# Performance work log

Hardware: AMD Instinct MI355X
Metric: run time of the kernel (lower is better)

Reference implementation:

```python
import jax, jax.numpy as jnp
import numpy as np

T = 4096      # tokens (flattened batch*seq)
DIN = 2048    # input hidden dim
DQ = 2048     # q output dim
DKV = 2048    # per-head-group kv output dim (== DQ here, MHA)
NA = 4        # number of adapters (LoRA/delta models)
R = 16        # lora rank per q/k/v


def setup_inputs() -> dict:
    key = jax.random.key(0)
    ks = jax.random.split(key, 8)
    def rn(k, shape, scale):
        return jax.random.normal(k, shape, dtype=jnp.float32) * scale
    return {
        "x": rn(ks[0], (T, DIN), 1.0),
        "W_base": rn(ks[1], (DQ + 2 * DKV, DIN), DIN ** -0.5),
        "A_buffer_qkv": rn(ks[2], (NA, DIN, 3 * R), DIN ** -0.5),
        "B_buffer_q": rn(ks[3], (NA, R, DQ), R ** -0.5),
        "B_buffer_kv": rn(ks[4], (NA, R, 2 * DKV), R ** -0.5),
        "DeltaW_q": rn(ks[5], (NA, DIN, DQ), DIN ** -0.5),
        "DeltaW_kv": rn(ks[6], (NA, DIN, 2 * DKV), DIN ** -0.5),
        "weight_indices": jax.random.randint(ks[7], (T,), 0, NA, dtype=jnp.int32),
    }


def _ldmm(indices, x, A, B, D):
    """Per-token adapter-indexed (LoRA + dense delta) matmul.
    indices: [T] int, x: [T, din], A: [na, din, r], B: [na, r, dout], D: [na, din, dout].
    out[t] = (x[t] @ A[a]) @ B[a] + x[t] @ D[a]  with a = indices[t].
    Implemented as masked GEMMs over the small fixed adapter set.
    """
    na = A.shape[0]
    out = jnp.zeros((x.shape[0], B.shape[2]), dtype=x.dtype)
    for a in range(na):  # small fixed loop over adapters
        xa = jnp.where((indices == a)[:, None], x, jnp.zeros((), x.dtype))
        out = out + (xa @ A[a]) @ B[a] + xa @ D[a]
    return out


def reference(x, W_base, A_buffer_qkv, B_buffer_q, B_buffer_kv,
              DeltaW_q, DeltaW_kv, weight_indices):
    # base QKV projection (ColumnParallelLinear, no bias): [T, dq + 2*dkv]
    base = x @ W_base.T
    rank = A_buffer_qkv.shape[2] // 3
    b_dim_q = B_buffer_q.shape[2]
    b_dim_kv = B_buffer_kv.shape[2] // 2
    d_dim_kv = DeltaW_kv.shape[2] // 2
    for i in range(3):  # q, k, v slices
        if i == 0:
            o = _ldmm(weight_indices, x,
                      A_buffer_qkv[:, :, :rank], B_buffer_q, DeltaW_q)
            base = base.at[:, :b_dim_q].add(o)
        else:
            o = _ldmm(weight_indices, x,
                      A_buffer_qkv[:, :, i * rank:(i + 1) * rank],
                      B_buffer_kv[:, :, (i - 1) * b_dim_kv:i * b_dim_kv],
                      DeltaW_kv[:, :, (i - 1) * d_dim_kv:i * d_dim_kv])
            base = base.at[:, i * b_dim_kv:(i + 1) * b_dim_kv].add(o)
    return base
```

## Files before the change

kernel.cpp:

```cpp
#include <hip/hip_runtime.h>
#include <stdint.h>

#define T_TOK 4096
#define DIN   2048
#define DQ    2048
#define DKV   2048
#define NOUT  (DQ + 2*DKV)
#define NA    4
#define RLORA 16
#define BM    256
#define BN    256
#define MPAD  (T_TOK + NA*BM)
#define MTILES (MPAD/BM)
#define KX    (DIN + 64)
#define NKT64 (KX/64)
#define KSPLIT 16
#define NTBLK (NOUT/BN)
#define NWG   (MTILES*NTBLK)

typedef unsigned short u16;
typedef __attribute__((ext_vector_type(8))) short short8;
typedef __attribute__((ext_vector_type(8))) u16 u16x8;
typedef __attribute__((ext_vector_type(4))) float f32x4;

__device__ __forceinline__ u16 f2bf(float f) {
  uint32_t u = __float_as_uint(f);
  u = (u + 0x7FFFu + ((u >> 16) & 1u)) >> 16;
  return (u16)u;
}
__device__ __forceinline__ float bf2f(u16 u) {
  return __uint_as_float(((uint32_t)u) << 16);
}

typedef __attribute__((address_space(3))) void lds_void;
typedef __attribute__((address_space(1))) void glb_void;

__device__ __forceinline__ void gl_lds16(const void* g, void* l) {
  __builtin_amdgcn_global_load_lds((const glb_void*)(uintptr_t)g,
                                   (lds_void*)(uint32_t)(uintptr_t)l, 16, 0, 0);
}

__global__ void prep_kernel(const int* __restrict__ widx,
                            int* __restrict__ tok,
                            int* __restrict__ tileAdapter) {
  __shared__ int cnt[256][NA];
  __shared__ int total[NA];
  __shared__ int pad_off[NA];
  const int tid = threadIdx.x;
  const int CH = T_TOK / 256;
  const int base = tid * CH;
  int c[NA] = {0, 0, 0, 0};
  for (int i = 0; i < CH; i++) c[widx[base + i]]++;
  for (int a = 0; a < NA; a++) cnt[tid][a] = c[a];
  __syncthreads();
  if (tid < NA) {
    int s = 0;
    for (int i = 0; i < 256; i++) { int v = cnt[i][tid]; cnt[i][tid] = s; s += v; }
    total[tid] = s;
  }
  __syncthreads();
  if (tid == 0) {
    int off = 0;
    for (int a = 0; a < NA; a++) {
      pad_off[a] = off;
      int ntile = (total[a] + BM - 1) / BM;
      for (int tl = 0; tl < ntile; tl++) tileAdapter[off / BM + tl] = a;
      off += ntile * BM;
    }
    for (int tl = off / BM; tl < MTILES; tl++) tileAdapter[tl] = -1;
  }
  __syncthreads();
  for (int i = tid; i < MPAD; i += 256) tok[i] = -1;
  __syncthreads();
  int myoff[NA];
  for (int a = 0; a < NA; a++) myoff[a] = pad_off[a] + cnt[tid][a];
  for (int i = 0; i < CH; i++) {
    int a = widx[base + i];
    tok[myoff[a]++] = base + i;
  }
}

__global__ void gather_kernel(const float* __restrict__ x,
                              const int* __restrict__ tok,
                              u16* __restrict__ Xg) {
  const int row = blockIdx.x;
  const int t = tok[row];
  const int tid = threadIdx.x;
  u16x8* dst = (u16x8*)(Xg + (size_t)row * KX);
  if (t < 0) {
    u16x8 z = {0, 0, 0, 0, 0, 0, 0, 0};
    dst[tid] = z;
    return;
  }
  const f32x4* src = (const f32x4*)(x + (size_t)t * DIN);
  f32x4 v0 = src[tid * 2];
  f32x4 v1 = src[tid * 2 + 1];
  u16x8 o;
  o[0] = f2bf(v0[0]); o[1] = f2bf(v0[1]); o[2] = f2bf(v0[2]); o[3] = f2bf(v0[3]);
  o[4] = f2bf(v1[0]); o[5] = f2bf(v1[1]); o[6] = f2bf(v1[2]); o[7] = f2bf(v1[3]);
  dst[tid] = o;
}

__global__ __launch_bounds__(256) void xa_partial_kernel(
    const u16* __restrict__ Xg, const float* __restrict__ A_qkv,
    const int* __restrict__ tileAdapter, float* __restrict__ Ppart) {
  const int ks = blockIdx.y;
  const int ad = tileAdapter[blockIdx.x >> 1];
  const int a = ad < 0 ? 0 : ad;
  const int kb = ks * (DIN / KSPLIT);
  const int tid = threadIdx.x;
  const int rg = tid >> 2;
  const int jg = tid & 3;
  const int r0 = blockIdx.x * 128 + rg * 2;
  const int j0 = jg * 12;
  __shared__ float ldsA[64][56];
  float acc[2][12];
  #pragma unroll
  for (int r = 0; r < 2; r++)
    #pragma unroll
    for (int j = 0; j < 12; j++) acc[r][j] = 0.f;

  for (int kc = 0; kc < 2; kc++) {
    const int kbase = kb + kc * 64;
    for (int i = tid; i < 64 * 48; i += 256) {
      int kk = i / 48, j = i - kk * 48;
      ldsA[kk][j] = A_qkv[((size_t)a * DIN + kbase + kk) * (3 * RLORA) + j];
    }
    __syncthreads();
    u16x8 xr[2][8];
    #pragma unroll
    for (int r = 0; r < 2; r++)
      #pragma unroll
      for (int q = 0; q < 8; q++)
        xr[r][q] = *(const u16x8*)(Xg + (size_t)(r0 + r) * KX + kbase + q * 8);
    #pragma unroll
    for (int q = 0; q < 8; q++) {
      #pragma unroll
      for (int e = 0; e < 8; e++) {
        const int kk = q * 8 + e;
        f32x4 a0 = *(const f32x4*)&ldsA[kk][j0];
        f32x4 a1 = *(const f32x4*)&ldsA[kk][j0 + 4];
        f32x4 a2 = *(const f32x4*)&ldsA[kk][j0 + 8];
        float x0 = bf2f(xr[0][q][e]);
        float x1 = bf2f(xr[1][q][e]);
        #pragma unroll
        for (int c = 0; c < 4; c++) {
          acc[0][c]     += x0 * a0[c];  acc[1][c]     += x1 * a0[c];
          acc[0][4 + c] += x0 * a1[c];  acc[1][4 + c] += x1 * a1[c];
          acc[0][8 + c] += x0 * a2[c];  acc[1][8 + c] += x1 * a2[c];
        }
      }
    }
    __syncthreads();
  }
  #pragma unroll
  for (int r = 0; r < 2; r++)
    #pragma unroll
    for (int j = 0; j < 12; j++)
      Ppart[((size_t)ks * MPAD + r0 + r) * 48 + j0 + j] = acc[r][j];
}

__global__ void xa_reduce_kernel(const float* __restrict__ Ppart,
                                 u16* __restrict__ Xg) {
  const int gid = blockIdx.x * 256 + threadIdx.x;
  const int row = gid >> 6, j = gid & 63;
  float s = 0.f;
  if (j < 48) {
    #pragma unroll
    for (int sp = 0; sp < KSPLIT; sp++)
      s += Ppart[((size_t)sp * MPAD + row) * 48 + j];
  }
  Xg[(size_t)row * KX + DIN + j] = f2bf(s);
}

__global__ __launch_bounds__(256) void weff2_kernel(
    const float* __restrict__ W_base,
    const float* __restrict__ DW_q, const float* __restrict__ DW_kv,
    u16* __restrict__ Weff) {
  const int k0 = blockIdx.x * 64;
  const int n0 = blockIdx.y * 64;
  const int tid = threadIdx.x;
  const int k8 = (tid & 7) * 8;
  __shared__ float ldsD[64][65];

  f32x4 wb[2][2];
  #pragma unroll
  for (int h = 0; h < 2; h++) {
    const int nn = h * 32 + (tid >> 3);
    const float* p = W_base + (size_t)(n0 + nn) * DIN + k0 + k8;
    wb[h][0] = *(const f32x4*)p;
    wb[h][1] = *(const f32x4*)(p + 4);
  }

  const int ldD  = (n0 < DQ) ? DQ : 2 * DKV;
  const int ncol = (n0 < DQ) ? n0 : n0 - DQ;
  const float* Dbase = (n0 < DQ) ? (DW_q + ncol) : (DW_kv + ncol);
  const size_t Dstride = (n0 < DQ) ? (size_t)DIN * DQ : (size_t)DIN * (2 * DKV);

  const int lkk = tid >> 6;
  const int lnn = tid & 63;

  float v[16];
  {
    const float* Dp = Dbase;
    #pragma unroll
    for (int j = 0; j < 16; j++)
      v[j] = Dp[(size_t)(k0 + lkk + 4 * j) * ldD + lnn];
  }

  for (int a = 0; a < NA; a++) {
    #pragma unroll
    for (int j = 0; j < 16; j++) ldsD[lkk + 4 * j][lnn] = v[j];
    if (a < NA - 1) {
      const float* Dp = Dbase + (size_t)(a + 1) * Dstride;
      #pragma unroll
      for (int j = 0; j < 16; j++)
        v[j] = Dp[(size_t)(k0 + lkk + 4 * j) * ldD + lnn];
    }
    __syncthreads();
    #pragma unroll
    for (int h = 0; h < 2; h++) {
      const int nn = h * 32 + (tid >> 3);
      u16x8 o;
      #pragma unroll
      for (int j = 0; j < 8; j++)
        o[j] = f2bf(wb[h][j >> 2][j & 3] + ldsD[k8 + j][nn]);
      *(u16x8*)(Weff + ((size_t)a * NOUT + n0 + nn) * KX + k0 + k8) = o;
    }
    __syncthreads();
  }
}

__global__ void wslots_kernel(const float* __restrict__ B_q,
                              const float* __restrict__ B_kv,
                              u16* __restrict__ Weff) {
  const int a = blockIdx.y;
  const int n = blockIdx.x * 256 + threadIdx.x;
  const int seg = n >> 11;
  u16 vals[64];
  #pragma unroll
  for (int j = 0; j < 64; j++) vals[j] = 0;
  if (seg == 0) {
    const float* Bp = B_q + ((size_t)a * RLORA) * DQ + n;
    #pragma unroll
    for (int r = 0; r < RLORA; r++) vals[r] = f2bf(Bp[(size_t)r * DQ]);
  } else if (seg == 1) {
    const float* Bp = B_kv + ((size_t)a * RLORA) * (2 * DKV) + (n - DQ);
    #pragma unroll
    for (int r = 0; r < RLORA; r++) vals[RLORA + r] = f2bf(Bp[(size_t)r * (2 * DKV)]);
  } else {
    const float* Bp = B_kv + ((size_t)a * RLORA) * (2 * DKV) + (n - DQ);
    #pragma unroll
    for (int r = 0; r < RLORA; r++) vals[2 * RLORA + r] = f2bf(Bp[(size_t)r * (2 * DKV)]);
  }
  u16* dst = Weff + ((size_t)a * NOUT + n) * KX + DIN;
  #pragma unroll
  for (int v = 0; v < 8; v++) *(u16x8*)(dst + v * 8) = *(u16x8*)(vals + v * 8);
}

#define BAR      asm volatile("s_barrier" ::: "memory")
#define WAITV(n) asm volatile("s_waitcnt vmcnt(" #n ")" ::: "memory")

#define RD_A(db, mh) { \
  _Pragma("unroll") for (int q = 0; q < 4; ++q) { \
    const char* rp = ldsc + (db)*32768 + (wm*128 + (mh)*64 + q*16 + fr)*128; \
    af[q][0] = *(const short8*)(rp + ck0); \
    af[q][1] = *(const short8*)(rp + ck1); } }

#define RD_B(db, nh, bfv) { \
  _Pragma("unroll") for (int q = 0; q < 2; ++q) { \
    const char* rp = ldsc + 65536 + (db)*32768 + ((nh)*128 + wn*32 + q*16 + fr)*128; \
    bfv[q][0] = *(const short8*)(rp + ck0); \
    bfv[q][1] = *(const short8*)(rp + ck1); } }

#define ST_A(db, mh, t) { \
  gl_lds16(gAsrc + (size_t)((mh)*64)*KX + (size_t)(t)*64, \
           ldsu + (db)*16384 + ((mh)*64*64) + stid); \
  gl_lds16(gAsrc + (size_t)(128 + (mh)*64)*KX + (size_t)(t)*64, \
           ldsu + (db)*16384 + ((128 + (mh)*64)*64) + stid); }

#define ST_B(db, nh, t) { \
  gl_lds16(gBsrc + (size_t)((nh)*32)*KX + (size_t)(t)*64, \
           ldsu + 32768 + (db)*16384 + ((nh)*128*64) + stid); \
  gl_lds16(gBsrc + (size_t)(128 + (nh)*32)*KX + (size_t)(t)*64, \
           ldsu + 32768 + (db)*16384 + (((nh)*128 + 64)*64) + stid); }

#define MM(mh, nh, bfv) { \
  __builtin_amdgcn_s_setprio(1); \
  _Pragma("unroll") for (int q = 0; q < 4; ++q) \
  _Pragma("unroll") for (int r = 0; r < 2; ++r) { \
    acc[(mh)*4+q][(nh)*2+r] = __builtin_amdgcn_mfma_f32_16x16x32_bf16( \
        af[q][0], bfv[r][0], acc[(mh)*4+q][(nh)*2+r], 0, 0, 0); \
    acc[(mh)*4+q][(nh)*2+r] = __builtin_amdgcn_mfma_f32_16x16x32_bf16( \
        af[q][1], bfv[r][1], acc[(mh)*4+q][(nh)*2+r], 0, 0, 0); } \
  __builtin_amdgcn_s_setprio(0); }

#define KT_STD(db, t) { \
  RD_A(db, 0); RD_B(db, 0, bf0); ST_A(1-(db), 1, (t)+1); BAR; MM(0, 0, bf0); BAR; \
  RD_B(db, 1, bf1);              ST_B(1-(db), 0, (t)+1); BAR; MM(0, 1, bf1); BAR; \
  RD_A(db, 1);                   ST_A(db, 0, (t)+2);     BAR; MM(1, 1, bf1); BAR; \
  ST_B(db, 1, (t)+2); WAITV(4);                          BAR; MM(1, 0, bf0); BAR; }

#define KT_T31(db, t) { \
  RD_A(db, 0); RD_B(db, 0, bf0); ST_A(1-(db), 1, (t)+1); BAR; MM(0, 0, bf0); BAR; \
  RD_B(db, 1, bf1);              ST_B(1-(db), 0, (t)+1); BAR; MM(0, 1, bf1); BAR; \
  RD_A(db, 1);                                           BAR; MM(1, 1, bf1); BAR; \
  WAITV(0);                                              BAR; MM(1, 0, bf0); BAR; }

#define KT_LAST(db) { \
  RD_A(db, 0); RD_B(db, 0, bf0); BAR; MM(0, 0, bf0); BAR; \
  RD_B(db, 1, bf1);              BAR; MM(0, 1, bf1); BAR; \
  RD_A(db, 1);                   BAR; MM(1, 1, bf1); BAR; \
                                 BAR; MM(1, 0, bf0); BAR; }

__global__ __launch_bounds__(512, 2) void gemm256_kernel(
    const u16* __restrict__ Xg, const u16* __restrict__ Weff,
    const int* __restrict__ tok, const int* __restrict__ tileAdapter,
    float* __restrict__ out) {
  __shared__ __align__(16) u16 Lds[65536];

  const int bid = blockIdx.x;
  const int lw = (bid & 7) * (NWG / 8) + (bid >> 3);
  const int pg  = lw / (2 * NTBLK);
  const int rem = lw % (2 * NTBLK);
  const int nt  = rem >> 1;
  const int mt  = pg * 2 + (rem & 1);
  const int a = tileAdapter[mt];
  if (a < 0) return;
  const int m0 = mt * BM, n0 = nt * BN;

  const int tid = threadIdx.x;
  const int l = tid & 63, w = tid >> 6;
  const int wm = w >> 2, wn = w & 3;
  const int fr = l & 15;
  const int kq = l >> 4;
  const int s7 = l & 7;
  const int ck0 = ((kq ^ s7) << 4);
  const int ck1 = (((4 + kq) ^ s7) << 4);

  const int l64 = tid >> 3;
  const int swc = (tid & 7) ^ (l64 & 7);
  const int stid = tid * 8;
  const u16* gAsrc = Xg + (size_t)(m0 + l64) * KX + swc * 8;
  const int nB = ((l64 >> 5) * 64) + (l64 & 31);
  const u16* gBsrc = Weff + ((size_t)a * NOUT + n0 + nB) * KX + swc * 8;

  u16* ldsu = &Lds[0];
  const char* ldsc = (const char*)ldsu;

  f32x4 acc[8][4];
  #pragma unroll
  for (int i = 0; i < 8; i++)
    #pragma unroll
    for (int j = 0; j < 4; j++) acc[i][j] = (f32x4){0.f, 0.f, 0.f, 0.f};

  short8 af[4][2], bf0[2][2], bf1[2][2];

  ST_A(0, 0, 0); ST_B(0, 0, 0); ST_A(0, 1, 0); ST_B(0, 1, 0);
  ST_A(1, 0, 1); ST_B(1, 1, 1);
  WAITV(4);
  BAR;

  for (int p = 0; p < 15; ++p) {
    const int t0 = 2 * p;
    KT_STD(0, t0);
    KT_STD(1, t0 + 1);
  }
  KT_STD(0, 30);
  KT_T31(1, 31);
  KT_LAST(0);

  #pragma unroll
  for (int mi = 0; mi < 8; ++mi) {
    const int rb = m0 + wm * 128 + mi * 16 + ((l >> 4) << 2);
    int tt[4];
    #pragma unroll
    for (int reg = 0; reg < 4; ++reg) tt[reg] = tok[rb + reg];
    #pragma unroll
    for (int ni = 0; ni < 4; ++ni) {
      const int col = n0 + wn * 64 + ni * 16 + fr;
      #pragma unroll
      for (int reg = 0; reg < 4; ++reg)
        if (tt[reg] >= 0) out[(size_t)tt[reg] * NOUT + col] = acc[mi][ni][reg];
    }
  }
}

__global__ void fallback_kernel(const float* __restrict__ x,
                                const float* __restrict__ W_base,
                                const float* __restrict__ A_qkv,
                                const float* __restrict__ B_q,
                                const float* __restrict__ B_kv,
                                const float* __restrict__ DW_q,
                                const float* __restrict__ DW_kv,
                                const int* __restrict__ widx,
                                float* __restrict__ out) {
  const int t = blockIdx.x;
  const int n = blockIdx.y * 256 + threadIdx.x;
  const int a = widx[t];
  __shared__ float xs[DIN];
  __shared__ float ys[3 * RLORA];
  for (int k = threadIdx.x; k < DIN; k += 256) xs[k] = x[(size_t)t * DIN + k];
  __syncthreads();
  if (threadIdx.x < 3 * RLORA) {
    float s = 0.f;
    const float* Ap = A_qkv + (size_t)a * DIN * (3 * RLORA) + threadIdx.x;
    for (int k = 0; k < DIN; k++) s += xs[k] * Ap[(size_t)k * (3 * RLORA)];
    ys[threadIdx.x] = s;
  }
  __syncthreads();
  const float* dcol; int ldD, roff; const float* bcol; int ldB;
  if (n < DQ) {
    dcol = DW_q + (size_t)a * DIN * DQ + n; ldD = DQ; roff = 0;
    bcol = B_q + (size_t)a * RLORA * DQ + n; ldB = DQ;
  } else {
    dcol = DW_kv + (size_t)a * DIN * (2 * DKV) + (n - DQ); ldD = 2 * DKV;
    roff = (n < 2 * DQ) ? RLORA : 2 * RLORA;
    bcol = B_kv + (size_t)a * RLORA * (2 * DKV) + (n - DQ); ldB = 2 * DKV;
  }
  const float* wrow = W_base + (size_t)n * DIN;
  float acc = 0.f;
  for (int k = 0; k < DIN; k++) acc += xs[k] * (wrow[k] + dcol[(size_t)k * ldD]);
  for (int r = 0; r < RLORA; r++) acc += ys[roff + r] * bcol[(size_t)r * ldB];
  out[(size_t)t * NOUT + n] = acc;
}

extern "C" void kernel_launch(void* const* d_in, const int* in_sizes, int n_in,
                              void* d_out, int out_size, void* d_ws, size_t ws_size,
                              hipStream_t stream) {
  const float* x      = (const float*)d_in[0];
  const float* W_base = (const float*)d_in[1];
  const float* A_qkv  = (const float*)d_in[2];
  const float* B_q    = (const float*)d_in[3];
  const float* B_kv   = (const float*)d_in[4];
  const float* DW_q   = (const float*)d_in[5];
  const float* DW_kv  = (const float*)d_in[6];
  const int*   widx   = (const int*)d_in[7];
  float* out = (float*)d_out;

  const size_t WEFF_BYTES = (size_t)NA * NOUT * KX * sizeof(u16);
  const size_t XG_BYTES   = (size_t)MPAD * KX * sizeof(u16);
  const size_t TOK_BYTES  = (size_t)MPAD * sizeof(int);
  const size_t TILE_BYTES = (size_t)MTILES * sizeof(int);
  const size_t need = WEFF_BYTES + XG_BYTES + TOK_BYTES + TILE_BYTES;

  if (ws_size < need) {
    fallback_kernel<<<dim3(T_TOK, NOUT / 256), 256, 0, stream>>>(
        x, W_base, A_qkv, B_q, B_kv, DW_q, DW_kv, widx, out);
    return;
  }

  char* ws = (char*)d_ws;
  u16* Weff = (u16*)ws;
  u16* Xg   = (u16*)(ws + WEFF_BYTES);
  int* tok  = (int*)(ws + WEFF_BYTES + XG_BYTES);
  int* tileAdapter = tok + MPAD;
  float* Ppart = (float*)ws;

  prep_kernel<<<1, 256, 0, stream>>>(widx, tok, tileAdapter);
  gather_kernel<<<MPAD, 256, 0, stream>>>(x, tok, Xg);
  xa_partial_kernel<<<dim3(MPAD / 128, KSPLIT), 256, 0, stream>>>(
      Xg, A_qkv, tileAdapter, Ppart);
  xa_reduce_kernel<<<MPAD * 64 / 256, 256, 0, stream>>>(Ppart, Xg);
  weff2_kernel<<<dim3(DIN / 64, NOUT / 64), 256, 0, stream>>>(
      W_base, DW_q, DW_kv, Weff);
  wslots_kernel<<<dim3(NOUT / 256, NA), 256, 0, stream>>>(B_q, B_kv, Weff);
  gemm256_kernel<<<dim3(NWG), 512, 0, stream>>>(
      Xg, Weff, tok, tileAdapter, out);
}
```

Baseline: 249.1 us.

## Switch GEMM main loop to K=32 tiles with 4-stage LDS ring buffer

```diff
diff --git a/kernel.cpp b/kernel.cpp
--- a/kernel.cpp
+++ b/kernel.cpp
@@ -13,7 +13,7 @@
 #define MPAD  (T_TOK + NA*BM)
 #define MTILES (MPAD/BM)
 #define KX    (DIN + 64)
-#define NKT64 (KX/64)
+#define NKT   (KX/32)
 #define KSPLIT 16
 #define NTBLK (NOUT/BN)
 #define NWG   (MTILES*NTBLK)
@@ -261,57 +261,49 @@
 #define BAR      asm volatile("s_barrier" ::: "memory")
 #define WAITV(n) asm volatile("s_waitcnt vmcnt(" #n ")" ::: "memory")
 
-#define RD_A(db, mh) { \
+#define RD_A4(b, mlo) { \
   _Pragma("unroll") for (int q = 0; q < 4; ++q) { \
-    const char* rp = ldsc + (db)*32768 + (wm*128 + (mh)*64 + q*16 + fr)*128; \
-    af[q][0] = *(const short8*)(rp + ck0); \
-    af[q][1] = *(const short8*)(rp + ck1); } }
-
-#define RD_B(db, nh, bfv) { \
-  _Pragma("unroll") for (int q = 0; q < 2; ++q) { \
-    const char* rp = ldsc + 65536 + (db)*32768 + ((nh)*128 + wn*32 + q*16 + fr)*128; \
-    bfv[q][0] = *(const short8*)(rp + ck0); \
-    bfv[q][1] = *(const short8*)(rp + ck1); } }
-
-#define ST_A(db, mh, t) { \
-  gl_lds16(gAsrc + (size_t)((mh)*64)*KX + (size_t)(t)*64, \
-           ldsu + (db)*16384 + ((mh)*64*64) + stid); \
-  gl_lds16(gAsrc + (size_t)(128 + (mh)*64)*KX + (size_t)(t)*64, \
-           ldsu + (db)*16384 + ((128 + (mh)*64)*64) + stid); }
-
-#define ST_B(db, nh, t) { \
-  gl_lds16(gBsrc + (size_t)((nh)*32)*KX + (size_t)(t)*64, \
-           ldsu + 32768 + (db)*16384 + ((nh)*128*64) + stid); \
-  gl_lds16(gBsrc + (size_t)(128 + (nh)*32)*KX + (size_t)(t)*64, \
-           ldsu + 32768 + (db)*16384 + (((nh)*128 + 64)*64) + stid); }
-
-#define MM(mh, nh, bfv) { \
+    const char* rp = ldsc + (b)*16384 + (wm*128 + ((mlo)+q)*16)*64; \
+    af[(mlo)+q] = *(const short8*)(rp + laneoff); } }
+
+#define RD_B4(b) { \
+  _Pragma("unroll") for (int q = 0; q < 4; ++q) { \
+    const char* rp = ldsc + 65536 + (b)*16384 + (wn*64 + q*16)*64; \
+    bfr[q] = *(const short8*)(rp + laneoff); } }
+
+#define ST_U01(b, t) { \
+  gl_lds16(gAsrc + (size_t)(t)*32, ldsu + (b)*8192 + stid); \
+  gl_lds16(gAsrc + (size_t)128*KX + (size_t)(t)*32, ldsu + (b)*8192 + 4096 + stid); }
+
+#define ST_U23(b, t) { \
+  gl_lds16(gBsrc + (size_t)(t)*32, ldsu + 32768 + (b)*8192 + stid); \
+  gl_lds16(gBsrc + (size_t)128*KX + (size_t)(t)*32, ldsu + 32768 + (b)*8192 + 4096 + stid); }
+
+#define MM4(mlo) { \
   __builtin_amdgcn_s_setprio(1); \
-  _Pragma("unroll") for (int q = 0; q < 4; ++q) \
-  _Pragma("unroll") for (int r = 0; r < 2; ++r) { \
-    acc[(mh)*4+q][(nh)*2+r] = __builtin_amdgcn_mfma_f32_16x16x32_bf16( \
-        af[q][0], bfv[r][0], acc[(mh)*4+q][(nh)*2+r], 0, 0, 0); \
-    acc[(mh)*4+q][(nh)*2+r] = __builtin_amdgcn_mfma_f32_16x16x32_bf16( \
-        af[q][1], bfv[r][1], acc[(mh)*4+q][(nh)*2+r], 0, 0, 0); } \
+  _Pragma("unroll") for (int mi = 0; mi < 4; ++mi) \
+  _Pragma("unroll") for (int ni = 0; ni < 4; ++ni) \
+    acc[(mlo)+mi][ni] = __builtin_amdgcn_mfma_f32_16x16x32_bf16( \
+        af[(mlo)+mi], bfr[ni], acc[(mlo)+mi][ni], 0, 0, 0); \
   __builtin_amdgcn_s_setprio(0); }
 
-#define KT_STD(db, t) { \
-  RD_A(db, 0); RD_B(db, 0, bf0); ST_A(1-(db), 1, (t)+1); BAR; MM(0, 0, bf0); BAR; \
-  RD_B(db, 1, bf1);              ST_B(1-(db), 0, (t)+1); BAR; MM(0, 1, bf1); BAR; \
-  RD_A(db, 1);                   ST_A(db, 0, (t)+2);     BAR; MM(1, 1, bf1); BAR; \
-  ST_B(db, 1, (t)+2); WAITV(4);                          BAR; MM(1, 0, bf0); BAR; }
-
-#define KT_T31(db, t) { \
-  RD_A(db, 0); RD_B(db, 0, bf0); ST_A(1-(db), 1, (t)+1); BAR; MM(0, 0, bf0); BAR; \
-  RD_B(db, 1, bf1);              ST_B(1-(db), 0, (t)+1); BAR; MM(0, 1, bf1); BAR; \
-  RD_A(db, 1);                                           BAR; MM(1, 1, bf1); BAR; \
-  WAITV(0);                                              BAR; MM(1, 0, bf0); BAR; }
-
-#define KT_LAST(db) { \
-  RD_A(db, 0); RD_B(db, 0, bf0); BAR; MM(0, 0, bf0); BAR; \
-  RD_B(db, 1, bf1);              BAR; MM(0, 1, bf1); BAR; \
-  RD_A(db, 1);                   BAR; MM(1, 1, bf1); BAR; \
-                                 BAR; MM(1, 0, bf0); BAR; }
+#define TILE(b, t, W) { \
+  W; BAR; \
+  RD_A4(b, 0); RD_B4(b); ST_U01(((b)+3)&3, (t)+3); \
+  BAR; \
+  MM4(0); \
+  RD_A4(b, 4); ST_U23(((b)+3)&3, (t)+3); \
+  BAR; \
+  MM4(4); }
+
+#define TILE_N(b, W) { \
+  W; BAR; \
+  RD_A4(b, 0); RD_B4(b); \
+  BAR; \
+  MM4(0); \
+  RD_A4(b, 4); \
+  BAR; \
+  MM4(4); }
 
 __global__ __launch_bounds__(512, 2) void gemm256_kernel(
     const u16* __restrict__ Xg, const u16* __restrict__ Weff,
@@ -333,17 +325,13 @@
   const int l = tid & 63, w = tid >> 6;
   const int wm = w >> 2, wn = w & 3;
   const int fr = l & 15;
-  const int kq = l >> 4;
-  const int s7 = l & 7;
-  const int ck0 = ((kq ^ s7) << 4);
-  const int ck1 = (((4 + kq) ^ s7) << 4);
-
-  const int l64 = tid >> 3;
-  const int swc = (tid & 7) ^ (l64 & 7);
+  const int laneoff = fr * 64 + ((((l >> 4) ^ ((fr >> 1) & 3))) << 4);
+
+  const int srow = tid >> 2;
+  const int scol = (((tid & 3) ^ ((tid >> 3) & 3))) * 8;
   const int stid = tid * 8;
-  const u16* gAsrc = Xg + (size_t)(m0 + l64) * KX + swc * 8;
-  const int nB = ((l64 >> 5) * 64) + (l64 & 31);
-  const u16* gBsrc = Weff + ((size_t)a * NOUT + n0 + nB) * KX + swc * 8;
+  const u16* gAsrc = Xg + (size_t)(m0 + srow) * KX + scol;
+  const u16* gBsrc = Weff + ((size_t)a * NOUT + n0 + srow) * KX + scol;
 
   u16* ldsu = &Lds[0];
   const char* ldsc = (const char*)ldsu;
@@ -354,21 +342,25 @@
     #pragma unroll
     for (int j = 0; j < 4; j++) acc[i][j] = (f32x4){0.f, 0.f, 0.f, 0.f};
 
-  short8 af[4][2], bf0[2][2], bf1[2][2];
-
-  ST_A(0, 0, 0); ST_B(0, 0, 0); ST_A(0, 1, 0); ST_B(0, 1, 0);
-  ST_A(1, 0, 1); ST_B(1, 1, 1);
-  WAITV(4);
-  BAR;
+  short8 af[8], bfr[4];
+
+  ST_U01(0, 0); ST_U23(0, 0);
+  ST_U01(1, 1); ST_U23(1, 1);
+  ST_U01(2, 2); ST_U23(2, 2);
 
   for (int p = 0; p < 15; ++p) {
-    const int t0 = 2 * p;
-    KT_STD(0, t0);
-    KT_STD(1, t0 + 1);
-  }
-  KT_STD(0, 30);
-  KT_T31(1, 31);
-  KT_LAST(0);
+    const int t4 = 4 * p;
+    TILE(0, t4 + 0, WAITV(8));
+    TILE(1, t4 + 1, WAITV(8));
+    TILE(2, t4 + 2, WAITV(8));
+    TILE(3, t4 + 3, WAITV(8));
+  }
+  TILE(0, 60, WAITV(8));
+  TILE(1, 61, WAITV(8));
+  TILE(2, 62, WAITV(8));
+  TILE_N(3, WAITV(8));
+  TILE_N(0, WAITV(4));
+  TILE_N(1, WAITV(0));
 
   #pragma unroll
   for (int mi = 0; mi < 8; ++mi) {
```

After: 257.4 us. 3.3% more time.
